# Optimization experiments

Hardware: AMD Instinct MI355X
Metric: run time of the kernel (lower is better)

Reference implementation:

```python
import jax, jax.numpy as jnp
import numpy as np

D_MODEL = 1024
N_HEAD = 16
D_HEAD = D_MODEL // N_HEAD
N_CTX = 2048
ROPE_BASE = 10000.0
SCALE = 1


def _rope_cache(seq_len, d_head, dtype=jnp.float32):
    inv_freq = 1.0 / (ROPE_BASE ** (jnp.arange(0, d_head, 2, dtype=jnp.float32) / d_head))
    t = jnp.arange(seq_len, dtype=jnp.float32)
    freqs = jnp.outer(t, inv_freq)              # [S, d_head/2]
    emb = jnp.concatenate([freqs, freqs], -1)   # [S, d_head]  (concat, per source)
    cos = jnp.cos(emb)[None, :, None, :].astype(dtype)
    sin = jnp.sin(emb)[None, :, None, :].astype(dtype)
    return cos, sin


def _apply_rope(x, cos, sin):
    # x: [B, S, H, Dh]; interleaved rotate (stack then flatten), per source
    x_even = x[..., 0::2]
    x_odd = x[..., 1::2]
    x_rot = jnp.stack([-x_odd, x_even], axis=-1).reshape(x.shape)
    return x * cos + x_rot * sin


def _rmsnorm(x, w):
    eps = jnp.finfo(x.dtype).eps  # torch RMSNorm default eps
    var = jnp.mean(jnp.square(x), axis=-1, keepdims=True)
    return x * jax.lax.rsqrt(var + eps) * w


def setup_inputs() -> dict:
    key = jax.random.key(0)
    ks = jax.random.split(key, 9)
    B, S = 2, N_CTX
    x = jax.random.normal(ks[0], (B, S, D_MODEL), jnp.float32)
    s = 0.02
    Wq = jax.random.normal(ks[1], (D_MODEL, D_MODEL), jnp.float32) * s
    bq = jax.random.normal(ks[2], (D_MODEL,), jnp.float32) * s
    Wk = jax.random.normal(ks[3], (D_MODEL, D_MODEL), jnp.float32) * s
    bk = jax.random.normal(ks[4], (D_MODEL,), jnp.float32) * s
    Wv = jax.random.normal(ks[5], (D_MODEL, D_MODEL), jnp.float32) * s
    bv = jax.random.normal(ks[6], (D_MODEL,), jnp.float32) * s
    Wo = jax.random.normal(ks[7], (D_MODEL, D_MODEL), jnp.float32) * s
    norm_w = jnp.ones((D_HEAD,), jnp.float32)
    return {"x": x, "Wq": Wq, "bq": bq, "Wk": Wk, "bk": bk,
            "Wv": Wv, "bv": bv, "Wo": Wo, "norm_w": norm_w}


def reference(x, Wq, bq, Wk, bk, Wv, bv, Wo, norm_w):
    B, S, _ = x.shape
    split = lambda t: t.reshape(B, S, N_HEAD, D_HEAD)
    q = split(x @ Wq.T + bq)
    k = split(x @ Wk.T + bk)
    v = split(x @ Wv.T + bv)
    cos, sin = _rope_cache(S, D_HEAD, x.dtype)
    q = _apply_rope(_rmsnorm(q, norm_w), cos, sin)
    k = _apply_rope(_rmsnorm(k, norm_w), cos, sin)
    scores = jnp.einsum('bqhd,bkhd->bhqk', q, k)
    causal = jnp.tril(jnp.ones((S, S), x.dtype))
    pattern = jnp.square(scores / D_HEAD) * causal  # quadratic score, masked
    z = jnp.einsum('bhqk,bkhd->bqhd', pattern, v).reshape(B, S, D_MODEL)
    return x + (z @ Wo.T) * SCALE
```

## Files before the change

kernel.cpp:

```cpp
#include <hip/hip_runtime.h>
#include <math.h>


typedef float  f32x4  __attribute__((ext_vector_type(4)));
typedef short  bf16x8 __attribute__((ext_vector_type(8)));
typedef float  vf4    __attribute__((ext_vector_type(4)));
typedef unsigned short u16x4 __attribute__((ext_vector_type(4)));

static __device__ __forceinline__ unsigned short f2bf(float f) {
    union { float f; unsigned int i; } c; c.f = f;
    unsigned int x = c.i;
    return (unsigned short)((x + 0x7fffu + ((x >> 16) & 1u)) >> 16);
}
static __device__ __forceinline__ f32x4 shfl_xor4(f32x4 v, int m) {
    f32x4 r;
    r[0] = __shfl_xor(v[0], m); r[1] = __shfl_xor(v[1], m);
    r[2] = __shfl_xor(v[2], m); r[3] = __shfl_xor(v[3], m);
    return r;
}
static __device__ __forceinline__ f32x4 rsq4(f32x4 v) {
    f32x4 r;
#pragma unroll
    for (int i = 0; i < 4; i++) r[i] = rsqrtf(v[i] * (1.0f / 64.0f) + 1.1920929e-07f);
    return r;
}
static __device__ __forceinline__ void cp16(const unsigned short* g, unsigned short* l) {
    __builtin_amdgcn_global_load_lds(
        (const __attribute__((address_space(1))) unsigned int*)g,
        (__attribute__((address_space(3))) unsigned int*)l, 16, 0, 0);
}

#define FOR_M(X)  X(0) X(1) X(2) X(3)
#define FOR_MN(X) X(0,0) X(0,1) X(0,2) X(0,3) X(1,0) X(1,1) X(1,2) X(1,3) \
                  X(2,0) X(2,1) X(2,2) X(2,3) X(3,0) X(3,1) X(3,2) X(3,3)

#define MF(c,a,b) c = __builtin_amdgcn_mfma_f32_16x16x32_bf16(a, b, c, 0, 0, 0);

#define VMC4 asm volatile("s_waitcnt vmcnt(4)" ::: "memory");
#define VMC0 asm volatile("s_waitcnt vmcnt(0)" ::: "memory");
#define LGC0 asm volatile("s_waitcnt lgkmcnt(0)" ::: "memory");
#define BARR __builtin_amdgcn_s_barrier();

__global__ __launch_bounds__(256) void cvt_all(
    const float* __restrict__ x,  const float* __restrict__ Wq,
    const float* __restrict__ Wk, const float* __restrict__ Wv,
    const float* __restrict__ Wo,
    unsigned short* __restrict__ xb,  unsigned short* __restrict__ Wqb,
    unsigned short* __restrict__ Wkb, unsigned short* __restrict__ Wvb,
    unsigned short* __restrict__ Wob, int nx4, int nw4)
{
    int i = blockIdx.x * 256 + threadIdx.x;
    const float* s; unsigned short* d; int li;
    if (i < nx4) { s = x; d = xb; li = i; }
    else {
        int idx = i - nx4;
        int r = idx / nw4; li = idx - r * nw4;
        if (r >= 4) return;
        s = (r == 0) ? Wq : (r == 1) ? Wk : (r == 2) ? Wv : Wo;
        d = (r == 0) ? Wqb : (r == 1) ? Wkb : (r == 2) ? Wvb : Wob;
    }
    vf4 v = *(const vf4*)(s + (size_t)li * 4);
    u16x4 o;
#pragma unroll
    for (int j = 0; j < 4; j++) o[j] = f2bf(v[j]);
    *(u16x4*)(d + (size_t)li * 4) = o;
}

#define SS 136

__global__ __launch_bounds__(256, 3) void gemm_qkvz(
    const unsigned short* __restrict__ xb,
    const unsigned short* __restrict__ Wqb,
    const unsigned short* __restrict__ Wkb,
    const unsigned short* __restrict__ Wvb,
    const float* __restrict__ bqf, const float* __restrict__ bkf, const float* __restrict__ bvf,
    const float* __restrict__ nwp,
    unsigned short* __restrict__ qb, unsigned short* __restrict__ kb,
    unsigned short* __restrict__ vT)
{
    const int K = 1024;
    __shared__ unsigned short smem[24576];
    const int lbid = blockIdx.x;
    const int wid_ = (lbid & 7) * 96 + (lbid >> 3);
    const int z = wid_ >> 8;
    const int rem = wid_ & 255;
    const int m0 = (rem >> 3) * 128;
    const int n0 = (rem & 7) * 128;
    const unsigned short* Wb = (z == 0) ? Wqb : (z == 1) ? Wkb : Wvb;
    const float* bias = (z == 0) ? bqf : (z == 1) ? bkf : bvf;
    const int tid = threadIdx.x;
    const int lane = tid & 63, wid = tid >> 6;
    const int wy = wid >> 1, wx = wid & 1;
    const int l15 = lane & 15, quad = lane >> 4;
    const int r16 = lane >> 2;
    const int c8  = (lane & 3) * 8;

#define Z_DECL_ACC(mi,ni) f32x4 c##mi##ni = {0.f, 0.f, 0.f, 0.f};
    FOR_MN(Z_DECL_ACC)

#define Z_STAGE(BUF, KT) { \
        unsigned short* dstb = smem + (BUF) * 8192; \
        _Pragma("unroll") \
        for (int j = 0; j < 4; j++) { \
            const int ch = wid * 4 + j;           \
            const int mat = ch >> 3;              \
            const int row = (ch & 7) * 16 + r16; \
            const unsigned short* g = mat \
                ? Wb + (size_t)(n0 + row) * K + (KT) + c8 \
                : xb + (size_t)(m0 + row) * K + (KT) + c8; \
            cp16(g, &dstb[ch * 512]); \
        } }

#define Z_COMPUTE(BUF) { \
        const unsigned short* As_ = smem + (BUF) * 8192; \
        const unsigned short* Bs_ = As_ + 4096; \
        const bf16x8 a0 = *(const bf16x8*)&As_[(wy * 64 +  0 + l15) * 32 + quad * 8]; \
        const bf16x8 a1 = *(const bf16x8*)&As_[(wy * 64 + 16 + l15) * 32 + quad * 8]; \
        const bf16x8 a2 = *(const bf16x8*)&As_[(wy * 64 + 32 + l15) * 32 + quad * 8]; \
        const bf16x8 a3 = *(const bf16x8*)&As_[(wy * 64 + 48 + l15) * 32 + quad * 8]; \
        const bf16x8 b0 = *(const bf16x8*)&Bs_[(wx * 64 +  0 + l15) * 32 + quad * 8]; \
        const bf16x8 b1 = *(const bf16x8*)&Bs_[(wx * 64 + 16 + l15) * 32 + quad * 8]; \
        const bf16x8 b2 = *(const bf16x8*)&Bs_[(wx * 64 + 32 + l15) * 32 + quad * 8]; \
        const bf16x8 b3 = *(const bf16x8*)&Bs_[(wx * 64 + 48 + l15) * 32 + quad * 8]; \
        MF(c00,a0,b0) MF(c01,a0,b1) MF(c02,a0,b2) MF(c03,a0,b3) \
        MF(c10,a1,b0) MF(c11,a1,b1) MF(c12,a1,b2) MF(c13,a1,b3) \
        MF(c20,a2,b0) MF(c21,a2,b1) MF(c22,a2,b2) MF(c23,a2,b3) \
        MF(c30,a3,b0) MF(c31,a3,b1) MF(c32,a3,b2) MF(c33,a3,b3) }

    Z_STAGE(0, 0)
    Z_STAGE(1, 32)
    for (int p = 0; p < 10; ++p) {
        const int t = p * 3;
        VMC4 BARR Z_STAGE(2, (t + 2) * 32) Z_COMPUTE(0) LGC0
        VMC4 BARR Z_STAGE(0, (t + 3) * 32) Z_COMPUTE(1) LGC0
        VMC4 BARR Z_STAGE(1, (t + 4) * 32) Z_COMPUTE(2) LGC0
    }
    VMC4 BARR Z_COMPUTE(0) LGC0
    VMC0 BARR Z_COMPUTE(1)
    __syncthreads();

    const float bs0 = bias[n0 + wx * 64 + l15];
    const float bs1 = bias[n0 + wx * 64 + 16 + l15];
    const float bs2 = bias[n0 + wx * 64 + 32 + l15];
    const float bs3 = bias[n0 + wx * 64 + 48 + l15];
#define Z_BIAS(mi) c##mi##0 += bs0; c##mi##1 += bs1; c##mi##2 += bs2; c##mi##3 += bs3;
    FOR_M(Z_BIAS)

    if (z < 2) {
        const float nww0 = nwp[l15],      nww1 = nwp[16 + l15];
        const float nww2 = nwp[32 + l15], nww3 = nwp[48 + l15];
        const float lf0 = expf(-(float)l15 * 0.28782313662425572f);
        const float lf1 = expf(-(float)(l15 + 16) * 0.28782313662425572f);

#define Z_S2(mi) f32x4 s2_##mi = c##mi##0*c##mi##0 + c##mi##1*c##mi##1 + \
                                 c##mi##2*c##mi##2 + c##mi##3*c##mi##3; \
        s2_##mi = s2_##mi + shfl_xor4(s2_##mi, 1); \
        s2_##mi = s2_##mi + shfl_xor4(s2_##mi, 2); \
        s2_##mi = s2_##mi + shfl_xor4(s2_##mi, 4); \
        s2_##mi = s2_##mi + shfl_xor4(s2_##mi, 8); \
        s2_##mi = rsq4(s2_##mi);
        FOR_M(Z_S2)

#define Z_ROPE_ONE(mi,ni,NW,CS,SN) { \
            float vn = c##mi##ni[r] * s2v[r] * NW; \
            float pt = __shfl_xor(vn, 1); \
            float rot = (lane & 1) ? pt : -pt; \
            smem[mrow * SS + wx * 64 + (ni) * 16 + l15] = f2bf((vn * (CS) + rot * (SN)) * 0.125f); }
#define Z_ROPE_MI(mi) { f32x4 s2v = s2_##mi; \
            _Pragma("unroll") \
            for (int r = 0; r < 4; r++) { \
                const int mrow = wy * 64 + (mi) * 16 + quad * 4 + r; \
                const float t = (float)((m0 + mrow) & 2047); \
                const float a0 = t * lf0, a1 = t * lf1; \
                const float cs0 = cosf(a0), sn0 = sinf(a0); \
                const float cs1 = cosf(a1), sn1 = sinf(a1); \
                Z_ROPE_ONE(mi,0,nww0,cs0,sn0) Z_ROPE_ONE(mi,1,nww1,cs1,sn1) \
                Z_ROPE_ONE(mi,2,nww2,cs0,sn0) Z_ROPE_ONE(mi,3,nww3,cs1,sn1) } }
        FOR_M(Z_ROPE_MI)

        __syncthreads();
        unsigned short* dst = z ? kb : qb;
#pragma unroll
        for (int it = 0; it < 8; it++) {
            const int linear = tid + it * 256;
            const int row = linear >> 4, cb = linear & 15;
            *(bf16x8*)(dst + (size_t)(m0 + row) * 1024 + n0 + cb * 8) =
                *(const bf16x8*)&smem[row * SS + cb * 8];
        }
    } else {
#define Z_VST(mi,ni) { _Pragma("unroll") \
            for (int r = 0; r < 4; r++) { \
                const int mrow = wy * 64 + (mi) * 16 + quad * 4 + r; \
                smem[(wx * 64 + (ni) * 16 + l15) * SS + mrow] = f2bf(c##mi##ni[r]); } }
        FOR_MN(Z_VST)
        __syncthreads();
        const int b = m0 >> 11, tok0 = m0 & 2047;
#pragma unroll
        for (int it = 0; it < 8; it++) {
            const int linear = tid + it * 256;
            const int rowd = linear >> 4, cb = linear & 15;
            const int head_g = (n0 >> 6) + (rowd >> 6);
            const int d = rowd & 63;
            *(bf16x8*)(vT + (((size_t)b * 16 + head_g) * 64 + d) * 2048 + tok0 + cb * 8) =
                *(const bf16x8*)&smem[rowd * SS + cb * 8];
        }
    }
}

__global__ __launch_bounds__(256, 3) void gemm_out(
    const unsigned short* __restrict__ zb,
    const unsigned short* __restrict__ Wob,
    const float* __restrict__ x, float* __restrict__ out, int M)
{
    const int K = 1024;
    __shared__ unsigned short smem[24576];
    const int tid = threadIdx.x;
    const int n0 = blockIdx.x * 128;
    const int m0 = blockIdx.y * 128;
    const int lane = tid & 63, wid = tid >> 6;
    const int wy = wid >> 1, wx = wid & 1;
    const int l15 = lane & 15, quad = lane >> 4;
    const int r16 = lane >> 2;
    const int c8  = (lane & 3) * 8;

#define G_DECL_ACC(mi,ni) f32x4 c##mi##ni = {0.f, 0.f, 0.f, 0.f};
    FOR_MN(G_DECL_ACC)

#define O_STAGE(BUF, KT) { \
        unsigned short* dstb = smem + (BUF) * 8192; \
        _Pragma("unroll") \
        for (int j = 0; j < 4; j++) { \
            const int ch = wid * 4 + j; \
            const int mat = ch >> 3; \
            const int row = (ch & 7) * 16 + r16; \
            const unsigned short* g = mat \
                ? Wob + (size_t)(n0 + row) * K + (KT) + c8 \
                : zb  + (size_t)(m0 + row) * K + (KT) + c8; \
            cp16(g, &dstb[ch * 512]); \
        } }

#define O_COMPUTE(BUF) { \
        const unsigned short* As_ = smem + (BUF) * 8192; \
        const unsigned short* Bs_ = As_ + 4096; \
        const bf16x8 a0 = *(const bf16x8*)&As_[(wy * 64 +  0 + l15) * 32 + quad * 8]; \
        const bf16x8 a1 = *(const bf16x8*)&As_[(wy * 64 + 16 + l15) * 32 + quad * 8]; \
        const bf16x8 a2 = *(const bf16x8*)&As_[(wy * 64 + 32 + l15) * 32 + quad * 8]; \
        const bf16x8 a3 = *(const bf16x8*)&As_[(wy * 64 + 48 + l15) * 32 + quad * 8]; \
        const bf16x8 b0 = *(const bf16x8*)&Bs_[(wx * 64 +  0 + l15) * 32 + quad * 8]; \
        const bf16x8 b1 = *(const bf16x8*)&Bs_[(wx * 64 + 16 + l15) * 32 + quad * 8]; \
        const bf16x8 b2 = *(const bf16x8*)&Bs_[(wx * 64 + 32 + l15) * 32 + quad * 8]; \
        const bf16x8 b3 = *(const bf16x8*)&Bs_[(wx * 64 + 48 + l15) * 32 + quad * 8]; \
        MF(c00,a0,b0) MF(c01,a0,b1) MF(c02,a0,b2) MF(c03,a0,b3) \
        MF(c10,a1,b0) MF(c11,a1,b1) MF(c12,a1,b2) MF(c13,a1,b3) \
        MF(c20,a2,b0) MF(c21,a2,b1) MF(c22,a2,b2) MF(c23,a2,b3) \
        MF(c30,a3,b0) MF(c31,a3,b1) MF(c32,a3,b2) MF(c33,a3,b3) }

    O_STAGE(0, 0)
    O_STAGE(1, 32)
    for (int p = 0; p < 10; ++p) {
        const int t = p * 3;
        VMC4 BARR O_STAGE(2, (t + 2) * 32) O_COMPUTE(0) LGC0
        VMC4 BARR O_STAGE(0, (t + 3) * 32) O_COMPUTE(1) LGC0
        VMC4 BARR O_STAGE(1, (t + 4) * 32) O_COMPUTE(2) LGC0
    }
    VMC4 BARR O_COMPUTE(0) LGC0
    VMC0 BARR O_COMPUTE(1)

#define G_OUTST(mi,ni) { _Pragma("unroll") \
        for (int r = 0; r < 4; r++) { \
            const int m = m0 + wy * 64 + (mi) * 16 + quad * 4 + r; \
            const int n = n0 + wx * 64 + (ni) * 16 + l15; \
            out[(size_t)m * 1024 + n] = c##mi##ni[r] + x[(size_t)m * 1024 + n]; } }
    FOR_MN(G_OUTST)
}

__global__ __launch_bounds__(256, 4) void attn_mfma(
    const unsigned short* __restrict__ qb, const unsigned short* __restrict__ kb,
    const unsigned short* __restrict__ vT, unsigned short* __restrict__ zb)
{
    __shared__ unsigned short Qs[64 * 72];
    __shared__ unsigned short Ks[64 * 72];
    __shared__ unsigned short Vs[64 * 72];
    __shared__ unsigned short Pm[64 * 72];
    const int tid = threadIdx.x;

    const int bid = blockIdx.x;
    const int halfsz = gridDim.x >> 1;
    const int half = (bid >= halfsz) ? 1 : 0;
    const int r = bid - half * halfsz;
    const int qt = half ? (r & 15) : 31 - (r & 15);
    const int bh = r >> 4;

    const int b = bh >> 4, h = bh & 15;
    const int lane = tid & 63, wq = tid >> 6;
    const int l15 = lane & 15, quad = lane >> 4;
    const size_t tokbase = (size_t)b * 2048;
    const int q0 = qt * 64;

#pragma unroll
    for (int j = 0; j < 2; j++) {
        const int u = tid + j * 256;
        const int row = u >> 3, seg = (u & 7) * 8;
        bf16x8 v = *(const bf16x8*)(qb + (tokbase + q0 + row) * 1024 + h * 64 + seg);
        *(bf16x8*)&Qs[row * 72 + seg] = v;
    }
    __syncthreads();
    const bf16x8 aq0 = *(const bf16x8*)&Qs[(wq * 16 + l15) * 72 + quad * 8];
    const bf16x8 aq1 = *(const bf16x8*)&Qs[(wq * 16 + l15) * 72 + 32 + quad * 8];

    const int kr = tid >> 3;
    const int sg = (tid & 7) * 8;

    bf16x8 pk0, pk1, pv0, pv1;
#define A_GLB(KT) { \
        pk0 = *(const bf16x8*)(kb + (tokbase + (KT) * 64 + kr) * 1024 + h * 64 + sg); \
        pk1 = *(const bf16x8*)(kb + (tokbase + (KT) * 64 + kr + 32) * 1024 + h * 64 + sg); \
        pv0 = *(const bf16x8*)(vT + ((size_t)bh * 64 + kr) * 2048 + (KT) * 64 + sg); \
        pv1 = *(const bf16x8*)(vT + ((size_t)bh * 64 + kr + 32) * 2048 + (KT) * 64 + sg); }

    f32x4 z_0 = {0.f,0.f,0.f,0.f}, z_1 = {0.f,0.f,0.f,0.f};
    f32x4 z_2 = {0.f,0.f,0.f,0.f}, z_3 = {0.f,0.f,0.f,0.f};

    const int nkt = qt + 1;
    A_GLB(0)
    for (int kt = 0; kt < nkt; kt++) {
        __syncthreads();
        *(bf16x8*)&Ks[kr * 72 + sg] = pk0;
        *(bf16x8*)&Ks[(kr + 32) * 72 + sg] = pk1;
        *(bf16x8*)&Vs[kr * 72 + sg] = pv0;
        *(bf16x8*)&Vs[(kr + 32) * 72 + sg] = pv1;
        __syncthreads();
        if (kt + 1 < nkt) A_GLB(kt + 1)

        f32x4 s_0 = {0.f,0.f,0.f,0.f}, s_1 = {0.f,0.f,0.f,0.f};
        f32x4 s_2 = {0.f,0.f,0.f,0.f}, s_3 = {0.f,0.f,0.f,0.f};
#define A_QKH(KS, AQ) { \
        bf16x8 b0 = *(const bf16x8*)&Ks[(l15) * 72 + (KS) * 32 + quad * 8]; \
        bf16x8 b1 = *(const bf16x8*)&Ks[(16 + l15) * 72 + (KS) * 32 + quad * 8]; \
        bf16x8 b2 = *(const bf16x8*)&Ks[(32 + l15) * 72 + (KS) * 32 + quad * 8]; \
        bf16x8 b3 = *(const bf16x8*)&Ks[(48 + l15) * 72 + (KS) * 32 + quad * 8]; \
        MF(s_0, AQ, b0) MF(s_1, AQ, b1) MF(s_2, AQ, b2) MF(s_3, AQ, b3) }
        __builtin_amdgcn_s_setprio(1);
        A_QKH(0, aq0)
        A_QKH(1, aq1)
        __builtin_amdgcn_s_setprio(0);

        const bool needmask = (kt == qt);
#define A_PSTORE(n) { \
        f32x4 p4 = s_##n * s_##n; \
        if (needmask) { _Pragma("unroll") \
            for (int r2 = 0; r2 < 4; r2++) \
                if (kt * 64 + (n) * 16 + l15 > q0 + wq * 16 + quad * 4 + r2) p4[r2] = 0.f; } \
        _Pragma("unroll") \
        for (int r2 = 0; r2 < 4; r2++) \
            Pm[(wq * 16 + quad * 4 + r2) * 72 + (n) * 16 + l15] = f2bf(p4[r2]); }
        A_PSTORE(0) A_PSTORE(1) A_PSTORE(2) A_PSTORE(3)

#define A_PVH(KS) { \
        bf16x8 ap = *(const bf16x8*)&Pm[(wq * 16 + l15) * 72 + (KS) * 32 + quad * 8]; \
        bf16x8 u0 = *(const bf16x8*)&Vs[(l15) * 72 + (KS) * 32 + quad * 8]; \
        bf16x8 u1 = *(const bf16x8*)&Vs[(16 + l15) * 72 + (KS) * 32 + quad * 8]; \
        bf16x8 u2 = *(const bf16x8*)&Vs[(32 + l15) * 72 + (KS) * 32 + quad * 8]; \
        bf16x8 u3 = *(const bf16x8*)&Vs[(48 + l15) * 72 + (KS) * 32 + quad * 8]; \
        MF(z_0, ap, u0) MF(z_1, ap, u1) MF(z_2, ap, u2) MF(z_3, ap, u3) }
        __builtin_amdgcn_s_setprio(1);
        A_PVH(0)
        A_PVH(1)
        __builtin_amdgcn_s_setprio(0);
    }

#define A_ZST(n) { _Pragma("unroll") \
        for (int r2 = 0; r2 < 4; r2++) \
            Pm[(wq * 16 + quad * 4 + r2) * 72 + (n) * 16 + l15] = f2bf(z_##n[r2]); }
    A_ZST(0) A_ZST(1) A_ZST(2) A_ZST(3)
#pragma unroll
    for (int it = 0; it < 2; it++) {
        const int linear = it * 64 + lane;
        const int row = linear >> 3, cb = linear & 7;
        *(bf16x8*)(zb + (tokbase + q0 + wq * 16 + row) * 1024 + h * 64 + cb * 8) =
            *(const bf16x8*)&Pm[(wq * 16 + row) * 72 + cb * 8];
    }
}

extern "C" void kernel_launch(void* const* d_in, const int* in_sizes, int n_in,
                              void* d_out, int out_size, void* d_ws, size_t ws_size,
                              hipStream_t stream)
{
    const float* x  = (const float*)d_in[0];
    const float* Wq = (const float*)d_in[1];
    const float* bq = (const float*)d_in[2];
    const float* Wk = (const float*)d_in[3];
    const float* bk = (const float*)d_in[4];
    const float* Wv = (const float*)d_in[5];
    const float* bv = (const float*)d_in[6];
    const float* Wo = (const float*)d_in[7];
    const float* nw = (const float*)d_in[8];
    float* out = (float*)d_out;

    const int D = 1024;
    const int M = in_sizes[0] / D;

    unsigned short* xbb = (unsigned short*)d_ws;
    unsigned short* Wqb = xbb + (size_t)M * D;
    unsigned short* Wkb = Wqb + (size_t)D * D;
    unsigned short* Wvb = Wkb + (size_t)D * D;
    unsigned short* Wob = Wvb + (size_t)D * D;
    unsigned short* qbw = Wob + (size_t)D * D;
    unsigned short* kbw = qbw + (size_t)M * D;
    unsigned short* vTw = kbw + (size_t)M * D;
    unsigned short* zbw = vTw + (size_t)M * D;

    const int nx4 = M * D / 4, nw4 = D * D / 4;
    const int ncvt = nx4 + 4 * nw4;
    cvt_all<<<(ncvt + 255) / 256, 256, 0, stream>>>(
        x, Wq, Wk, Wv, Wo, xbb, Wqb, Wkb, Wvb, Wob, nx4, nw4);

    gemm_qkvz<<<dim3(768), 256, 0, stream>>>(
        xbb, Wqb, Wkb, Wvb, bq, bk, bv, nw, qbw, kbw, vTw);

    attn_mfma<<<dim3((M / 2048) * 16 * 32), 256, 0, stream>>>(qbw, kbw, vTw, zbw);

    gemm_out<<<dim3(D / 128, M / 128), 256, 0, stream>>>(zbw, Wob, x, out, M);
}
```

Before: 185.5 us.

## Load GEMM A operand directly into registers, stage only weights in LDS

In the QKV projection GEMM, the activation (A) tiles are now read straight from global memory into registers, double-buffered across even and odd steps. Only the weight (B) tiles still go through the triple-buffered LDS pipeline. This cuts LDS footprint and LDS traffic for A and changes the waitcnt schedule to vmcnt(2). In exchange, the two waves that share A rows now fetch them twice from global memory and hold more registers.

Result: slower. 216.4 us (+16.7%).

```diff
diff --git a/kernel.cpp b/kernel.cpp
--- a/kernel.cpp
+++ b/kernel.cpp
@@ -37,6 +37,7 @@
 #define MF(c,a,b) c = __builtin_amdgcn_mfma_f32_16x16x32_bf16(a, b, c, 0, 0, 0);
 
 #define VMC4 asm volatile("s_waitcnt vmcnt(4)" ::: "memory");
+#define VMC2 asm volatile("s_waitcnt vmcnt(2)" ::: "memory");
 #define VMC0 asm volatile("s_waitcnt vmcnt(0)" ::: "memory");
 #define LGC0 asm volatile("s_waitcnt lgkmcnt(0)" ::: "memory");
 #define BARR __builtin_amdgcn_s_barrier();
@@ -79,7 +80,7 @@
     unsigned short* __restrict__ vT)
 {
     const int K = 1024;
-    __shared__ unsigned short smem[24576];
+    __shared__ unsigned short smem[17408];
     const int lbid = blockIdx.x;
     const int wid_ = (lbid & 7) * 96 + (lbid >> 3);
     const int z = wid_ >> 8;
@@ -92,51 +93,69 @@
     const int lane = tid & 63, wid = tid >> 6;
     const int wy = wid >> 1, wx = wid & 1;
     const int l15 = lane & 15, quad = lane >> 4;
-    const int r16 = lane >> 2;
-    const int c8  = (lane & 3) * 8;
 
 #define Z_DECL_ACC(mi,ni) f32x4 c##mi##ni = {0.f, 0.f, 0.f, 0.f};
     FOR_MN(Z_DECL_ACC)
 
-#define Z_STAGE(BUF, KT) { \
-        unsigned short* dstb = smem + (BUF) * 8192; \
+    const unsigned short* ab0 = xb + (size_t)(m0 + wy * 64 + l15) * K + quad * 8;
+    const unsigned short* ab1 = ab0 + (size_t)16 * K;
+    const unsigned short* ab2 = ab0 + (size_t)32 * K;
+    const unsigned short* ab3 = ab0 + (size_t)48 * K;
+
+    bf16x8 aE0, aE1, aE2, aE3, aO0, aO1, aO2, aO3;
+
+#define Z_ALOAD(P, T) \
+        a##P##0 = *(const bf16x8*)(ab0 + (T) * 32); \
+        a##P##1 = *(const bf16x8*)(ab1 + (T) * 32); \
+        a##P##2 = *(const bf16x8*)(ab2 + (T) * 32); \
+        a##P##3 = *(const bf16x8*)(ab3 + (T) * 32);
+
+#define Z_BSTAGE(BUF, T) { \
+        unsigned short* dstb = smem + (BUF) * 4096; \
         _Pragma("unroll") \
-        for (int j = 0; j < 4; j++) { \
-            const int ch = wid * 4 + j;           \
-            const int mat = ch >> 3;              \
-            const int row = (ch & 7) * 16 + r16; \
-            const unsigned short* g = mat \
-                ? Wb + (size_t)(n0 + row) * K + (KT) + c8 \
-                : xb + (size_t)(m0 + row) * K + (KT) + c8; \
-            cp16(g, &dstb[ch * 512]); \
+        for (int j = 0; j < 2; j++) { \
+            const int u = tid + j * 256; \
+            const int row = u >> 2, ch = u & 3; \
+            cp16(Wb + (size_t)(n0 + row) * K + (T) * 32 + ch * 8, &dstb[u * 8]); \
         } }
 
-#define Z_COMPUTE(BUF) { \
-        const unsigned short* As_ = smem + (BUF) * 8192; \
-        const unsigned short* Bs_ = As_ + 4096; \
-        const bf16x8 a0 = *(const bf16x8*)&As_[(wy * 64 +  0 + l15) * 32 + quad * 8]; \
-        const bf16x8 a1 = *(const bf16x8*)&As_[(wy * 64 + 16 + l15) * 32 + quad * 8]; \
-        const bf16x8 a2 = *(const bf16x8*)&As_[(wy * 64 + 32 + l15) * 32 + quad * 8]; \
-        const bf16x8 a3 = *(const bf16x8*)&As_[(wy * 64 + 48 + l15) * 32 + quad * 8]; \
+#define Z_COMPUTE(BUF, P) { \
+        const unsigned short* Bs_ = smem + (BUF) * 4096; \
         const bf16x8 b0 = *(const bf16x8*)&Bs_[(wx * 64 +  0 + l15) * 32 + quad * 8]; \
         const bf16x8 b1 = *(const bf16x8*)&Bs_[(wx * 64 + 16 + l15) * 32 + quad * 8]; \
         const bf16x8 b2 = *(const bf16x8*)&Bs_[(wx * 64 + 32 + l15) * 32 + quad * 8]; \
         const bf16x8 b3 = *(const bf16x8*)&Bs_[(wx * 64 + 48 + l15) * 32 + quad * 8]; \
-        MF(c00,a0,b0) MF(c01,a0,b1) MF(c02,a0,b2) MF(c03,a0,b3) \
-        MF(c10,a1,b0) MF(c11,a1,b1) MF(c12,a1,b2) MF(c13,a1,b3) \
-        MF(c20,a2,b0) MF(c21,a2,b1) MF(c22,a2,b2) MF(c23,a2,b3) \
-        MF(c30,a3,b0) MF(c31,a3,b1) MF(c32,a3,b2) MF(c33,a3,b3) }
-
-    Z_STAGE(0, 0)
-    Z_STAGE(1, 32)
-    for (int p = 0; p < 10; ++p) {
-        const int t = p * 3;
-        VMC4 BARR Z_STAGE(2, (t + 2) * 32) Z_COMPUTE(0) LGC0
-        VMC4 BARR Z_STAGE(0, (t + 3) * 32) Z_COMPUTE(1) LGC0
-        VMC4 BARR Z_STAGE(1, (t + 4) * 32) Z_COMPUTE(2) LGC0
-    }
-    VMC4 BARR Z_COMPUTE(0) LGC0
-    VMC0 BARR Z_COMPUTE(1)
+        MF(c00,a##P##0,b0) MF(c01,a##P##0,b1) MF(c02,a##P##0,b2) MF(c03,a##P##0,b3) \
+        MF(c10,a##P##1,b0) MF(c11,a##P##1,b1) MF(c12,a##P##1,b2) MF(c13,a##P##1,b3) \
+        MF(c20,a##P##2,b0) MF(c21,a##P##2,b1) MF(c22,a##P##2,b2) MF(c23,a##P##2,b3) \
+        MF(c30,a##P##3,b0) MF(c31,a##P##3,b1) MF(c32,a##P##3,b2) MF(c33,a##P##3,b3) }
+
+#define Z_STEP(BC, BS, CP, NP, T) \
+        VMC2 BARR \
+        Z_ALOAD(NP, (T) + 1) \
+        Z_BSTAGE(BS, (T) + 2) \
+        Z_COMPUTE(BC, CP) \
+        LGC0
+
+    Z_ALOAD(E, 0)
+    Z_BSTAGE(0, 0)
+    Z_BSTAGE(1, 1)
+
+    for (int p = 0; p < 5; ++p) {
+        const int T = p * 6;
+        Z_STEP(0, 2, E, O, T + 0)
+        Z_STEP(1, 0, O, E, T + 1)
+        Z_STEP(2, 1, E, O, T + 2)
+        Z_STEP(0, 2, O, E, T + 3)
+        Z_STEP(1, 0, E, O, T + 4)
+        Z_STEP(2, 1, O, E, T + 5)
+    }
+    VMC2 BARR
+    Z_ALOAD(O, 31)
+    Z_COMPUTE(0, E)
+    LGC0
+    VMC0 BARR
+    Z_COMPUTE(1, O)
     __syncthreads();
 
     const float bs0 = bias[n0 + wx * 64 + l15];
```

## Use two waves per block with 128x64 per-wave tiles in QKV GEMM

Applied to the files above, without the earlier changes.

Restructures the QKV projection GEMM from 4 waves of 64x64 sub-tiles to 2 waves, each covering 128x64 of the 128x128 block tile. Each wave now holds 32 accumulators and reuses its B fragments across 8 A fragments, which raises MFMA work per LDS read. Staging, the waitcnt depth and the epilogue loops are adjusted to match. In exchange, register pressure roughly doubles, the occupancy hint is dropped, and fewer waves are available to hide latency.

After: 253.1 us. 1.36x slower.

```diff
diff --git a/kernel.cpp b/kernel.cpp
--- a/kernel.cpp
+++ b/kernel.cpp
@@ -31,11 +31,13 @@
 }
 
 #define FOR_M(X)  X(0) X(1) X(2) X(3)
+#define FOR_M8(X) X(0) X(1) X(2) X(3) X(4) X(5) X(6) X(7)
 #define FOR_MN(X) X(0,0) X(0,1) X(0,2) X(0,3) X(1,0) X(1,1) X(1,2) X(1,3) \
                   X(2,0) X(2,1) X(2,2) X(2,3) X(3,0) X(3,1) X(3,2) X(3,3)
 
 #define MF(c,a,b) c = __builtin_amdgcn_mfma_f32_16x16x32_bf16(a, b, c, 0, 0, 0);
 
+#define VMC8 asm volatile("s_waitcnt vmcnt(8)" ::: "memory");
 #define VMC4 asm volatile("s_waitcnt vmcnt(4)" ::: "memory");
 #define VMC0 asm volatile("s_waitcnt vmcnt(0)" ::: "memory");
 #define LGC0 asm volatile("s_waitcnt lgkmcnt(0)" ::: "memory");
@@ -68,7 +70,7 @@
 
 #define SS 136
 
-__global__ __launch_bounds__(256, 3) void gemm_qkvz(
+__global__ __launch_bounds__(128) void gemm_qkvz(
     const unsigned short* __restrict__ xb,
     const unsigned short* __restrict__ Wqb,
     const unsigned short* __restrict__ Wkb,
@@ -89,53 +91,60 @@
     const unsigned short* Wb = (z == 0) ? Wqb : (z == 1) ? Wkb : Wvb;
     const float* bias = (z == 0) ? bqf : (z == 1) ? bkf : bvf;
     const int tid = threadIdx.x;
-    const int lane = tid & 63, wid = tid >> 6;
-    const int wy = wid >> 1, wx = wid & 1;
+    const int lane = tid & 63, wx = tid >> 6;
     const int l15 = lane & 15, quad = lane >> 4;
-    const int r16 = lane >> 2;
-    const int c8  = (lane & 3) * 8;
-
-#define Z_DECL_ACC(mi,ni) f32x4 c##mi##ni = {0.f, 0.f, 0.f, 0.f};
-    FOR_MN(Z_DECL_ACC)
-
-#define Z_STAGE(BUF, KT) { \
+
+#define Z_DECL_ACC(mi) f32x4 c##mi##0 = {0.f,0.f,0.f,0.f}, c##mi##1 = {0.f,0.f,0.f,0.f}, \
+                              c##mi##2 = {0.f,0.f,0.f,0.f}, c##mi##3 = {0.f,0.f,0.f,0.f};
+    FOR_M8(Z_DECL_ACC)
+
+#define Z_STAGE(BUF, T) { \
         unsigned short* dstb = smem + (BUF) * 8192; \
         _Pragma("unroll") \
-        for (int j = 0; j < 4; j++) { \
-            const int ch = wid * 4 + j;           \
-            const int mat = ch >> 3;              \
-            const int row = (ch & 7) * 16 + r16; \
+        for (int j = 0; j < 8; j++) { \
+            const int u = tid + j * 128; \
+            const int mat = u >> 9; \
+            const int row = (u >> 2) & 127; \
+            const int ch = u & 3; \
             const unsigned short* g = mat \
-                ? Wb + (size_t)(n0 + row) * K + (KT) + c8 \
-                : xb + (size_t)(m0 + row) * K + (KT) + c8; \
-            cp16(g, &dstb[ch * 512]); \
+                ? Wb + (size_t)(n0 + row) * K + (T) * 32 + ch * 8 \
+                : xb + (size_t)(m0 + row) * K + (T) * 32 + ch * 8; \
+            cp16(g, &dstb[u * 8]); \
         } }
 
 #define Z_COMPUTE(BUF) { \
         const unsigned short* As_ = smem + (BUF) * 8192; \
         const unsigned short* Bs_ = As_ + 4096; \
-        const bf16x8 a0 = *(const bf16x8*)&As_[(wy * 64 +  0 + l15) * 32 + quad * 8]; \
-        const bf16x8 a1 = *(const bf16x8*)&As_[(wy * 64 + 16 + l15) * 32 + quad * 8]; \
-        const bf16x8 a2 = *(const bf16x8*)&As_[(wy * 64 + 32 + l15) * 32 + quad * 8]; \
-        const bf16x8 a3 = *(const bf16x8*)&As_[(wy * 64 + 48 + l15) * 32 + quad * 8]; \
         const bf16x8 b0 = *(const bf16x8*)&Bs_[(wx * 64 +  0 + l15) * 32 + quad * 8]; \
         const bf16x8 b1 = *(const bf16x8*)&Bs_[(wx * 64 + 16 + l15) * 32 + quad * 8]; \
         const bf16x8 b2 = *(const bf16x8*)&Bs_[(wx * 64 + 32 + l15) * 32 + quad * 8]; \
         const bf16x8 b3 = *(const bf16x8*)&Bs_[(wx * 64 + 48 + l15) * 32 + quad * 8]; \
+        const bf16x8 a0 = *(const bf16x8*)&As_[(  0 + l15) * 32 + quad * 8]; \
+        const bf16x8 a1 = *(const bf16x8*)&As_[( 16 + l15) * 32 + quad * 8]; \
+        const bf16x8 a2 = *(const bf16x8*)&As_[( 32 + l15) * 32 + quad * 8]; \
+        const bf16x8 a3 = *(const bf16x8*)&As_[( 48 + l15) * 32 + quad * 8]; \
         MF(c00,a0,b0) MF(c01,a0,b1) MF(c02,a0,b2) MF(c03,a0,b3) \
         MF(c10,a1,b0) MF(c11,a1,b1) MF(c12,a1,b2) MF(c13,a1,b3) \
         MF(c20,a2,b0) MF(c21,a2,b1) MF(c22,a2,b2) MF(c23,a2,b3) \
-        MF(c30,a3,b0) MF(c31,a3,b1) MF(c32,a3,b2) MF(c33,a3,b3) }
+        MF(c30,a3,b0) MF(c31,a3,b1) MF(c32,a3,b2) MF(c33,a3,b3) \
+        const bf16x8 a4 = *(const bf16x8*)&As_[( 64 + l15) * 32 + quad * 8]; \
+        const bf16x8 a5 = *(const bf16x8*)&As_[( 80 + l15) * 32 + quad * 8]; \
+        const bf16x8 a6 = *(const bf16x8*)&As_[( 96 + l15) * 32 + quad * 8]; \
+        const bf16x8 a7 = *(const bf16x8*)&As_[(112 + l15) * 32 + quad * 8]; \
+        MF(c40,a4,b0) MF(c41,a4,b1) MF(c42,a4,b2) MF(c43,a4,b3) \
+        MF(c50,a5,b0) MF(c51,a5,b1) MF(c52,a5,b2) MF(c53,a5,b3) \
+        MF(c60,a6,b0) MF(c61,a6,b1) MF(c62,a6,b2) MF(c63,a6,b3) \
+        MF(c70,a7,b0) MF(c71,a7,b1) MF(c72,a7,b2) MF(c73,a7,b3) }
 
     Z_STAGE(0, 0)
-    Z_STAGE(1, 32)
+    Z_STAGE(1, 1)
     for (int p = 0; p < 10; ++p) {
         const int t = p * 3;
-        VMC4 BARR Z_STAGE(2, (t + 2) * 32) Z_COMPUTE(0) LGC0
-        VMC4 BARR Z_STAGE(0, (t + 3) * 32) Z_COMPUTE(1) LGC0
-        VMC4 BARR Z_STAGE(1, (t + 4) * 32) Z_COMPUTE(2) LGC0
-    }
-    VMC4 BARR Z_COMPUTE(0) LGC0
+        VMC8 BARR Z_STAGE(2, t + 2) Z_COMPUTE(0) LGC0
+        VMC8 BARR Z_STAGE(0, t + 3) Z_COMPUTE(1) LGC0
+        VMC8 BARR Z_STAGE(1, t + 4) Z_COMPUTE(2) LGC0
+    }
+    VMC8 BARR Z_COMPUTE(0) LGC0
     VMC0 BARR Z_COMPUTE(1)
     __syncthreads();
 
@@ -144,7 +153,7 @@
     const float bs2 = bias[n0 + wx * 64 + 32 + l15];
     const float bs3 = bias[n0 + wx * 64 + 48 + l15];
 #define Z_BIAS(mi) c##mi##0 += bs0; c##mi##1 += bs1; c##mi##2 += bs2; c##mi##3 += bs3;
-    FOR_M(Z_BIAS)
+    FOR_M8(Z_BIAS)
 
     if (z < 2) {
         const float nww0 = nwp[l15],      nww1 = nwp[16 + l15];
@@ -159,7 +168,7 @@
         s2_##mi = s2_##mi + shfl_xor4(s2_##mi, 4); \
         s2_##mi = s2_##mi + shfl_xor4(s2_##mi, 8); \
         s2_##mi = rsq4(s2_##mi);
-        FOR_M(Z_S2)
+        FOR_M8(Z_S2)
 
 #define Z_ROPE_ONE(mi,ni,NW,CS,SN) { \
             float vn = c##mi##ni[r] * s2v[r] * NW; \
@@ -169,35 +178,38 @@
 #define Z_ROPE_MI(mi) { f32x4 s2v = s2_##mi; \
             _Pragma("unroll") \
             for (int r = 0; r < 4; r++) { \
-                const int mrow = wy * 64 + (mi) * 16 + quad * 4 + r; \
+                const int mrow = (mi) * 16 + quad * 4 + r; \
                 const float t = (float)((m0 + mrow) & 2047); \
                 const float a0 = t * lf0, a1 = t * lf1; \
                 const float cs0 = cosf(a0), sn0 = sinf(a0); \
                 const float cs1 = cosf(a1), sn1 = sinf(a1); \
                 Z_ROPE_ONE(mi,0,nww0,cs0,sn0) Z_ROPE_ONE(mi,1,nww1,cs1,sn1) \
                 Z_ROPE_ONE(mi,2,nww2,cs0,sn0) Z_ROPE_ONE(mi,3,nww3,cs1,sn1) } }
-        FOR_M(Z_ROPE_MI)
+        FOR_M8(Z_ROPE_MI)
 
         __syncthreads();
         unsigned short* dst = z ? kb : qb;
 #pragma unroll
-        for (int it = 0; it < 8; it++) {
-            const int linear = tid + it * 256;
+        for (int it = 0; it < 16; it++) {
+            const int linear = tid + it * 128;
             const int row = linear >> 4, cb = linear & 15;
             *(bf16x8*)(dst + (size_t)(m0 + row) * 1024 + n0 + cb * 8) =
                 *(const bf16x8*)&smem[row * SS + cb * 8];
         }
     } else {
-#define Z_VST(mi,ni) { _Pragma("unroll") \
+#define Z_VST(mi) { _Pragma("unroll") \
             for (int r = 0; r < 4; r++) { \
-                const int mrow = wy * 64 + (mi) * 16 + quad * 4 + r; \
-                smem[(wx * 64 + (ni) * 16 + l15) * SS + mrow] = f2bf(c##mi##ni[r]); } }
-        FOR_MN(Z_VST)
+                const int mrow = (mi) * 16 + quad * 4 + r; \
+                smem[(wx * 64 +  0 + l15) * SS + mrow] = f2bf(c##mi##0[r]); \
+                smem[(wx * 64 + 16 + l15) * SS + mrow] = f2bf(c##mi##1[r]); \
+                smem[(wx * 64 + 32 + l15) * SS + mrow] = f2bf(c##mi##2[r]); \
+                smem[(wx * 64 + 48 + l15) * SS + mrow] = f2bf(c##mi##3[r]); } }
+        FOR_M8(Z_VST)
         __syncthreads();
         const int b = m0 >> 11, tok0 = m0 & 2047;
 #pragma unroll
-        for (int it = 0; it < 8; it++) {
-            const int linear = tid + it * 256;
+        for (int it = 0; it < 16; it++) {
+            const int linear = tid + it * 128;
             const int rowd = linear >> 4, cb = linear & 15;
             const int head_g = (n0 >> 6) + (rowd >> 6);
             const int d = rowd & 63;
@@ -415,7 +427,7 @@
     cvt_all<<<(ncvt + 255) / 256, 256, 0, stream>>>(
         x, Wq, Wk, Wv, Wo, xbb, Wqb, Wkb, Wvb, Wob, nx4, nw4);
 
-    gemm_qkvz<<<dim3(768), 256, 0, stream>>>(
+    gemm_qkvz<<<dim3(768), 128, 0, stream>>>(
         xbb, Wqb, Wkb, Wvb, bq, bk, bv, nw, qbw, kbw, vTw);
 
     attn_mfma<<<dim3((M / 2048) * 16 * 32), 256, 0, stream>>>(qbw, kbw, vTw, zbw);
```
